# Optimization experiments

Measured on AMD Instinct MI355X. Metric: run time of the kernel, lower is better.

Reference implementation:

```python
import jax, jax.numpy as jnp
import numpy as np

N_NODES = 50000
N_EDGES = 800000
D_IN, D_HID, D_OUT = 128, 256, 128
N_EXPERT = 8


def mean_aggr(x, src, dst, n):
    # scatter-mean of neighbor features onto destination nodes
    msg = x[src]                                            # [E, d]
    s = jax.ops.segment_sum(msg, dst, num_segments=n)       # [N, d]
    cnt = jax.ops.segment_sum(jnp.ones((src.shape[0],), x.dtype), dst, num_segments=n)
    return s / jnp.clip(cnt, 1.0)[:, None]


def moe_top1(x, wg, bg, we, be):
    # FMoE with naive gate, top_k=1: combine weight softmax over top-1 == 1.0
    logits = x @ wg + bg                                    # [N, E]
    gate_full = jax.nn.softmax(logits, axis=-1)             # [N, E]
    idx = jnp.argmax(logits, axis=-1)                       # [N]
    n_expert = we.shape[0]
    out = jnp.zeros((x.shape[0], we.shape[2]), x.dtype)
    for e in range(n_expert):                               # small fixed loop over experts
        mask = (idx == e)[:, None].astype(x.dtype)
        out = out + mask * (x @ we[e] + be[e])
    return out, gate_full


def mysage_conv(x, src, dst, wg, bg, we, be, wr):
    agg = mean_aggr(x, src, dst, x.shape[0])
    out, gate = moe_top1(agg, wg, bg, we, be)
    out = out + x @ wr                                      # root weight (no bias)
    gstd = jnp.std(gate, axis=1, ddof=1).mean()             # torch.std is unbiased
    return out, gstd


def plain_sage_conv(x, src, dst, wl, bl, wr):
    agg = mean_aggr(x, src, dst, x.shape[0])
    return agg @ wl + bl + x @ wr


def setup_inputs() -> dict:
    key = jax.random.key(0)
    ks = jax.random.split(key, 16)
    s = 0.05
    inp = {
        "x": jax.random.normal(ks[0], (N_NODES, D_IN), jnp.float32),
        "edge_index": jax.random.randint(ks[1], (2, N_EDGES), 0, N_NODES, jnp.int64),
        # layer 1 (in -> hid)
        "wg1": jax.random.normal(ks[2], (D_IN, N_EXPERT), jnp.float32) * s,
        "bg1": jnp.zeros((N_EXPERT,), jnp.float32),
        "we1": jax.random.normal(ks[3], (N_EXPERT, D_IN, D_HID), jnp.float32) * s,
        "be1": jnp.zeros((N_EXPERT, D_HID), jnp.float32),
        "wr1": jax.random.normal(ks[4], (D_IN, D_HID), jnp.float32) * s,
        # layer 2 (hid -> hid)
        "wg2": jax.random.normal(ks[5], (D_HID, N_EXPERT), jnp.float32) * s,
        "bg2": jnp.zeros((N_EXPERT,), jnp.float32),
        "we2": jax.random.normal(ks[6], (N_EXPERT, D_HID, D_HID), jnp.float32) * s,
        "be2": jnp.zeros((N_EXPERT, D_HID), jnp.float32),
        "wr2": jax.random.normal(ks[7], (D_HID, D_HID), jnp.float32) * s,
        # layer 3 plain SAGEConv (hid -> out)
        "wl3": jax.random.normal(ks[8], (D_HID, D_OUT), jnp.float32) * s,
        "bl3": jnp.zeros((D_OUT,), jnp.float32),
        "wr3": jax.random.normal(ks[9], (D_HID, D_OUT), jnp.float32) * s,
    }
    return inp


def reference(x, edge_index, wg1, bg1, we1, be1, wr1, wg2, bg2, we2, be2, wr2, wl3, bl3, wr3):
    src, dst = edge_index[0], edge_index[1]
    h, g1 = mysage_conv(x, src, dst, wg1, bg1, we1, be1, wr1)
    h = jax.nn.relu(h)                                      # dropout p=0 / eval mode
    h, g2 = mysage_conv(h, src, dst, wg2, bg2, we2, be2, wr2)
    h = jax.nn.relu(h)
    out = plain_sage_conv(h, src, dst, wl3, bl3, wr3)
    gate_std_mean = jnp.stack([g1, g2]).mean()
    return out, gate_std_mean
```

## Files before the change

kernel.cpp:

```cpp
#include <hip/hip_runtime.h>
#include <hip/hip_bf16.h>
#include <stdint.h>

#define DEV static __device__ __forceinline__

typedef __attribute__((ext_vector_type(8))) short short8;
typedef __attribute__((ext_vector_type(4))) float f32x4;

DEV float bf2f(unsigned short u) { return __uint_as_float(((unsigned)u) << 16); }
DEV float bflo(unsigned u) { return __uint_as_float(u << 16); }
DEV float bfhi(unsigned u) { return __uint_as_float(u & 0xffff0000u); }
DEV unsigned short f2bf(float f) {
    unsigned u = __float_as_uint(f);
    u += 0x7fff + ((u >> 16) & 1);
    return (unsigned short)(u >> 16);
}

__global__ void k_detect(const int* __restrict__ ei, int* __restrict__ flags) {
    if (threadIdx.x == 0 && blockIdx.x == 0) {
        int zeros = 0;
        for (int i = 0; i < 128; ++i) if (ei[2 * i + 1] == 0) ++zeros;
        flags[1] = (zeros >= 64) ? 1 : 0;
    }
}

__global__ void k_cvt_idx(const int* __restrict__ ei, int* __restrict__ src32,
                          int* __restrict__ dst32, int* __restrict__ deg,
                          int E, const int* __restrict__ flags) {
    int i = blockIdx.x * 256 + threadIdx.x;
    if (i >= E) return;
    int s, d;
    if (flags[1]) { s = ei[2 * i]; d = ei[2 * E + 2 * i]; }
    else          { s = ei[i];     d = ei[E + i]; }
    src32[i] = s; dst32[i] = d;
    atomicAdd(&deg[d], 1);
}

__global__ void k_transpose_nb(const float* __restrict__ in, unsigned short* __restrict__ out,
                               int R, int C) {
    __shared__ unsigned short tile[32][33];
    int tx = threadIdx.x & 31, ty = threadIdx.x >> 5;
    size_t mat = (size_t)blockIdx.z * R * C;
    int r0 = blockIdx.y * 32, c0 = blockIdx.x * 32;
#pragma unroll
    for (int j = 0; j < 32; j += 8)
        tile[ty + j][tx] = f2bf(in[mat + (size_t)(r0 + ty + j) * C + c0 + tx]);
    __syncthreads();
#pragma unroll
    for (int j = 0; j < 32; j += 8)
        out[mat + (size_t)(c0 + ty + j) * R + r0 + tx] = tile[tx][ty + j];
}

__global__ void k_bias3(const float* __restrict__ bl3, float* __restrict__ bias3) {
    int t = threadIdx.x;
    bias3[t] = (t < 128) ? 0.f : bl3[t - 128];
}

__global__ void k_scan1(const int* __restrict__ deg, int* __restrict__ row_ptr,
                        int* __restrict__ part, int n) {
    __shared__ int wsum[4];
    int t = threadIdx.x, lane = t & 63, wv = t >> 6;
    int i = blockIdx.x * 256 + t;
    int v0 = (i < n) ? deg[i] : 0;
    int v = v0;
#pragma unroll
    for (int d = 1; d < 64; d <<= 1) { int u = __shfl_up(v, d); if (lane >= d) v += u; }
    if (lane == 63) wsum[wv] = v;
    __syncthreads();
    int add = 0;
    for (int w2 = 0; w2 < wv; ++w2) add += wsum[w2];
    v += add;
    if (i < n) row_ptr[i] = v - v0;
    if (t == 255) part[blockIdx.x] = v;
}

__global__ void k_scan2(int* __restrict__ part, int P) {
    __shared__ int wsum[4];
    int t = threadIdx.x, lane = t & 63, wv = t >> 6;
    int v0 = (t < P) ? part[t] : 0;
    int v = v0;
#pragma unroll
    for (int d = 1; d < 64; d <<= 1) { int u = __shfl_up(v, d); if (lane >= d) v += u; }
    if (lane == 63) wsum[wv] = v;
    __syncthreads();
    int add = 0;
    for (int w2 = 0; w2 < wv; ++w2) add += wsum[w2];
    v += add;
    if (t < P) part[t] = v - v0;
}

__global__ void k_scan3(int* __restrict__ row_ptr, const int* __restrict__ part, int n, int E) {
    int i = blockIdx.x * 256 + threadIdx.x;
    if (i < n) row_ptr[i] += part[blockIdx.x];
    if (i == 0) row_ptr[n] = E;
}

__global__ void k_fill(const int* __restrict__ src, const int* __restrict__ dst,
                       const int* __restrict__ row_ptr, int* __restrict__ cursor,
                       int* __restrict__ csr, int E) {
    int i = blockIdx.x * 256 + threadIdx.x;
    if (i < E) {
        int d = dst[i];
        int p = atomicAdd(&cursor[d], 1);
        csr[row_ptr[d] + p] = src[i];
    }
}

template<int D>
__global__ void k_aggr(const float* __restrict__ xin, const int* __restrict__ row_ptr,
                       const int* __restrict__ csr, float* __restrict__ agg, int n) {
    int wid = (blockIdx.x * blockDim.x + threadIdx.x) >> 6;
    int lane = threadIdx.x & 63;
    if (wid >= n) return;
    constexpr int V = D / 64;
    double a0[V], a1[V], a2[V], a3[V];
#pragma unroll
    for (int i = 0; i < V; ++i) { a0[i] = 0.0; a1[i] = 0.0; a2[i] = 0.0; a3[i] = 0.0; }
    int s0 = row_ptr[wid], s1 = row_ptr[wid + 1];
    int j = s0;
    for (; j + 4 <= s1; j += 4) {
        int i0 = csr[j], i1 = csr[j + 1], i2 = csr[j + 2], i3 = csr[j + 3];
        const float* p0 = xin + (size_t)i0 * D + lane * V;
        const float* p1 = xin + (size_t)i1 * D + lane * V;
        const float* p2 = xin + (size_t)i2 * D + lane * V;
        const float* p3 = xin + (size_t)i3 * D + lane * V;
        if (V == 2) {
            float2 f0 = *(const float2*)p0, f1 = *(const float2*)p1;
            float2 f2 = *(const float2*)p2, f3 = *(const float2*)p3;
            a0[0] += (double)f0.x; a0[1] += (double)f0.y;
            a1[0] += (double)f1.x; a1[1] += (double)f1.y;
            a2[0] += (double)f2.x; a2[1] += (double)f2.y;
            a3[0] += (double)f3.x; a3[1] += (double)f3.y;
        } else {
            float4 f0 = *(const float4*)p0, f1 = *(const float4*)p1;
            float4 f2 = *(const float4*)p2, f3 = *(const float4*)p3;
            a0[0] += (double)f0.x; a0[1] += (double)f0.y; a0[2] += (double)f0.z; a0[3] += (double)f0.w;
            a1[0] += (double)f1.x; a1[1] += (double)f1.y; a1[2] += (double)f1.z; a1[3] += (double)f1.w;
            a2[0] += (double)f2.x; a2[1] += (double)f2.y; a2[2] += (double)f2.z; a2[3] += (double)f2.w;
            a3[0] += (double)f3.x; a3[1] += (double)f3.y; a3[2] += (double)f3.z; a3[3] += (double)f3.w;
        }
    }
    for (; j < s1; ++j) {
        const float* p = xin + (size_t)csr[j] * D + lane * V;
        if (V == 2) {
            float2 f = *(const float2*)p;
            a0[0] += (double)f.x; a0[1] += (double)f.y;
        } else {
            float4 f = *(const float4*)p;
            a0[0] += (double)f.x; a0[1] += (double)f.y; a0[2] += (double)f.z; a0[3] += (double)f.w;
        }
    }
    double inv = 1.0 / (double)max(s1 - s0, 1);
#pragma unroll
    for (int i = 0; i < V; ++i)
        agg[(size_t)wid * D + lane * V + i] = (float)(((a0[i] + a1[i]) + (a2[i] + a3[i])) * inv);
}

__global__ void k_aggr_badd(const unsigned short* __restrict__ Pb, const int* __restrict__ row_ptr,
                            const int* __restrict__ csr, const float* __restrict__ Rf,
                            float* __restrict__ outp, int n) {
    int wid = (blockIdx.x * blockDim.x + threadIdx.x) >> 6;
    int lane = threadIdx.x & 63;
    if (wid >= n) return;
    double a0[2], a1[2], a2[2], a3[2];
#pragma unroll
    for (int i = 0; i < 2; ++i) { a0[i] = 0.0; a1[i] = 0.0; a2[i] = 0.0; a3[i] = 0.0; }
    int s0 = row_ptr[wid], s1 = row_ptr[wid + 1];
    int j = s0;
    for (; j + 4 <= s1; j += 4) {
        int i0 = csr[j], i1 = csr[j + 1], i2 = csr[j + 2], i3 = csr[j + 3];
        unsigned u0 = *(const unsigned*)(Pb + (size_t)i0 * 128 + lane * 2);
        unsigned u1 = *(const unsigned*)(Pb + (size_t)i1 * 128 + lane * 2);
        unsigned u2 = *(const unsigned*)(Pb + (size_t)i2 * 128 + lane * 2);
        unsigned u3 = *(const unsigned*)(Pb + (size_t)i3 * 128 + lane * 2);
        a0[0] += (double)bflo(u0); a0[1] += (double)bfhi(u0);
        a1[0] += (double)bflo(u1); a1[1] += (double)bfhi(u1);
        a2[0] += (double)bflo(u2); a2[1] += (double)bfhi(u2);
        a3[0] += (double)bflo(u3); a3[1] += (double)bfhi(u3);
    }
    for (; j < s1; ++j) {
        unsigned u = *(const unsigned*)(Pb + (size_t)csr[j] * 128 + lane * 2);
        a0[0] += (double)bflo(u); a0[1] += (double)bfhi(u);
    }
    double inv = 1.0 / (double)max(s1 - s0, 1);
    float2 r = *(const float2*)(Rf + (size_t)wid * 128 + lane * 2);
    float2 o;
    o.x = (float)(((a0[0] + a1[0]) + (a2[0] + a3[0])) * inv) + r.x;
    o.y = (float)(((a0[1] + a1[1]) + (a2[1] + a3[1])) * inv) + r.y;
    *(float2*)(outp + (size_t)wid * 128 + lane * 2) = o;
}

template<int D>
__global__ void k_gate(const float* __restrict__ agg, const float* __restrict__ wg,
                       const float* __restrict__ bg, int* __restrict__ idx,
                       int* __restrict__ ecnt, float* __restrict__ gsum, int n) {
    __shared__ float swg[D * 8];
    __shared__ int hcnt[8];
    __shared__ float red[256];
    int t = threadIdx.x;
    if (t < 8) hcnt[t] = 0;
    for (int i = t; i < D * 8; i += 256) swg[i] = wg[i];
    __syncthreads();
    int nid = blockIdx.x * 256 + t;
    float stdv = 0.f;
    if (nid < n) {
        double lg[8];
#pragma unroll
        for (int e = 0; e < 8; ++e) lg[e] = (double)bg[e];
        const float* ap = agg + (size_t)nid * D;
        for (int k = 0; k < D; k += 4) {
            float4 a = *(const float4*)(ap + k);
#pragma unroll
            for (int e = 0; e < 8; ++e) {
                lg[e] += (double)a.x * swg[(k + 0) * 8 + e] + (double)a.y * swg[(k + 1) * 8 + e]
                       + (double)a.z * swg[(k + 2) * 8 + e] + (double)a.w * swg[(k + 3) * 8 + e];
            }
        }
        double m = lg[0];
        int am = 0;
#pragma unroll
        for (int e = 1; e < 8; ++e) if (lg[e] > m) { m = lg[e]; am = e; }
        double s = 0.0, p[8];
#pragma unroll
        for (int e = 0; e < 8; ++e) { p[e] = exp(lg[e] - m); s += p[e]; }
        double invs = 1.0 / s, sq = 0.0;
#pragma unroll
        for (int e = 0; e < 8; ++e) { double q = p[e] * invs; sq += q * q; }
        stdv = (float)sqrt(fmax(sq - 0.125, 0.0) / 7.0);
        idx[nid] = am;
        atomicAdd(&hcnt[am], 1);
    }
    red[t] = stdv;
    __syncthreads();
    for (int off = 128; off > 0; off >>= 1) {
        if (t < off) red[t] += red[t + off];
        __syncthreads();
    }
    if (t == 0) atomicAdd(gsum, red[0]);
    if (t < 8 && hcnt[t] > 0) atomicAdd(&ecnt[t], hcnt[t]);
}

__global__ void k_offsets(const int* __restrict__ ecnt, int* __restrict__ eoff) {
    if (threadIdx.x == 0 && blockIdx.x == 0) {
        int s = 0;
        for (int e = 0; e < 8; ++e) { eoff[e] = s; s += ecnt[e]; }
        eoff[8] = s;
    }
}

__global__ void k_perm(const int* __restrict__ idx, const int* __restrict__ eoff,
                       int* __restrict__ ecur, int* __restrict__ perm, int n) {
    __shared__ int lcnt[8], lbase[8];
    int t = threadIdx.x;
    if (t < 8) lcnt[t] = 0;
    __syncthreads();
    int nid = blockIdx.x * 256 + t;
    int e = 0, r = 0;
    bool valid = (nid < n);
    if (valid) { e = idx[nid]; r = atomicAdd(&lcnt[e], 1); }
    __syncthreads();
    if (t < 8) lbase[t] = lcnt[t] ? atomicAdd(&ecur[t], lcnt[t]) : 0;
    __syncthreads();
    if (valid) perm[eoff[e] + lbase[e] + r] = nid;
}

template<int NCOL, bool LOAD>
DEV void g_step(int g, const float* __restrict__ Bp, const float* __restrict__ at,
                float4 (&cur)[4], float (&acc)[8][4]) {
    float bx[4][4];
#pragma unroll
    for (int kk = 0; kk < 4; ++kk) {
        bx[kk][0] = cur[kk].x; bx[kk][1] = cur[kk].y;
        bx[kk][2] = cur[kk].z; bx[kk][3] = cur[kk].w;
    }
#pragma unroll
    for (int r = 0; r < 8; ++r) {
        float4 a = *(const float4*)(at + r * 68 + g * 4);
#pragma unroll
        for (int c = 0; c < 4; ++c) {
            acc[r][c] = fmaf(a.x, bx[0][c], acc[r][c]);
            acc[r][c] = fmaf(a.y, bx[1][c], acc[r][c]);
            acc[r][c] = fmaf(a.z, bx[2][c], acc[r][c]);
            acc[r][c] = fmaf(a.w, bx[3][c], acc[r][c]);
        }
    }
    if (LOAD) {
#pragma unroll
        for (int kk = 0; kk < 4; ++kk)
            cur[kk] = *(const float4*)(Bp + (size_t)(g * 4 + 8 + kk) * NCOL);
    }
}

template<int NCOL>
DEV void compute_chunk(const float* __restrict__ Bp, const float* __restrict__ at,
                       float (&acc)[8][4]) {
    float4 bA[4], bB[4];
#pragma unroll
    for (int kk = 0; kk < 4; ++kk) bA[kk] = *(const float4*)(Bp + (size_t)kk * NCOL);
#pragma unroll
    for (int kk = 0; kk < 4; ++kk) bB[kk] = *(const float4*)(Bp + (size_t)(4 + kk) * NCOL);
#pragma unroll 1
    for (int g = 0; g < 14; g += 2) {
        g_step<NCOL, true>(g, Bp, at, bA, acc);
        g_step<NCOL, true>(g + 1, Bp, at, bB, acc);
    }
    g_step<NCOL, false>(14, Bp, at, bA, acc);
    g_step<NCOL, false>(15, Bp, at, bB, acc);
}

template<int DIN, int NCOL, bool RELU>
__global__ __launch_bounds__(256, 4) void k_gemm_f32(
    const float* __restrict__ agg, const float* __restrict__ a2,
    const float* __restrict__ B1, const float* __restrict__ B2,
    const float* __restrict__ bias,
    const int* __restrict__ perm, const int* __restrict__ eoff,
    float* __restrict__ outp, int n) {
    static_assert(DIN == 128 && NCOL == 256, "layer-1 geometry");
    __shared__ float a_tile[2][4 * 8 * 68];
    __shared__ int rows[32];
    int t = threadIdx.x;
    int rs = blockIdx.x * 32;
    if (rs >= n) return;
    int nrows = min(32, n - rs);
    if (t < 32) rows[t] = perm[rs + min(t, nrows - 1)];
    __syncthreads();

    int e0 = 0, e1 = 0;
    int last = rs + nrows - 1;
#pragma unroll
    for (int e = 1; e < 8; ++e) {
        int v = eoff[e];
        if (v <= rs) e0 = e;
        if (v <= last) e1 = e;
    }
    int ne = e1 - e0 + 1;
    int nchunks = 2 * ne + 2;

    int lane = t & 63, rg = t >> 6;
    int cols = lane * 4;
    int srow = lane >> 3;
    int sk = (lane & 7) * 8;
    int gpos = rs + rg * 8 + srow;
    int myrow = rows[rg * 8 + srow];
    float* stc = &a_tile[0][rg * 544 + srow * 68 + sk];
    float* stn = &a_tile[1][rg * 544 + srow * 68 + sk];
    const float* atc = &a_tile[0][rg * 544];
    const float* atn = &a_tile[1][rg * 544];

    float acc[8][4];
#pragma unroll
    for (int r = 0; r < 8; ++r) { acc[r][0] = 0.f; acc[r][1] = 0.f; acc[r][2] = 0.f; acc[r][3] = 0.f; }

    auto params = [&](int c, const float*& ap, const float*& Bp, float& m) {
        int half = c & 1;
        if (c < 2 * ne) {
            int e = e0 + (c >> 1);
            ap = agg + (size_t)myrow * DIN + sk + half * 64;
            Bp = B1 + (size_t)e * DIN * NCOL + (size_t)half * 64 * NCOL + cols;
            m = (gpos >= eoff[e] && gpos < eoff[e + 1]) ? 1.f : 0.f;
        } else {
            ap = a2 + (size_t)myrow * DIN + sk + half * 64;
            Bp = B2 + (size_t)half * 64 * NCOL + cols;
            m = 1.f;
        }
    };

    const float* ap; const float* Bp; float m;
    params(0, ap, Bp, m);
    float4 p0 = *(const float4*)ap, p1 = *(const float4*)(ap + 4);
#pragma unroll 1
    for (int c = 0; c < nchunks; ++c) {
        float4 s0 = p0, s1 = p1;
        s0.x *= m; s0.y *= m; s0.z *= m; s0.w *= m;
        s1.x *= m; s1.y *= m; s1.z *= m; s1.w *= m;
        *(float4*)stc = s0; *(float4*)(stc + 4) = s1;
        const float* Bcur = Bp;
        if (c + 1 < nchunks) {
            params(c + 1, ap, Bp, m);
            p0 = *(const float4*)ap; p1 = *(const float4*)(ap + 4);
        }
        compute_chunk<NCOL>(Bcur, atc, acc);
        float* ts = stc; stc = stn; stn = ts;
        const float* ta = atc; atc = atn; atn = ta;
    }

#pragma unroll
    for (int r = 0; r < 8; ++r) {
        int rr = rg * 8 + r;
        if (rr < nrows) {
            int gp = rs + rr;
            int er = e0;
            for (int e = e0 + 1; e <= e1; ++e) if (eoff[e] <= gp) er = e;
            float4 bb = *(const float4*)(bias + er * NCOL + cols);
            int gr = rows[rr];
            float v0 = acc[r][0] + bb.x, v1 = acc[r][1] + bb.y;
            float v2 = acc[r][2] + bb.z, v3 = acc[r][3] + bb.w;
            if (RELU) { v0 = fmaxf(v0, 0.f); v1 = fmaxf(v1, 0.f); v2 = fmaxf(v2, 0.f); v3 = fmaxf(v3, 0.f); }
            *(float4*)(outp + (size_t)gr * NCOL + cols) = make_float4(v0, v1, v2, v3);
        }
    }
}

template<int DIN, int MODE, int CT>
DEV void gemm_half(const void* __restrict__ Asrc, const unsigned short* __restrict__ BT,
                   short (*Ah)[40], short (*Bs)[40],
                   const int* rows, f32x4 (&acc)[4][CT], int t, int lane, int w) {
    if (MODE == 9) return;
    int q = lane >> 4, m16 = lane & 15;
    int r = t >> 2, part = t & 3;
    for (int kc = 0; kc < DIN; kc += 32) {
        __syncthreads();
        if (MODE == 2) {
            *(uint4*)&Ah[r][part * 8] =
                *(const uint4*)((const unsigned short*)Asrc + (size_t)rows[r] * DIN + kc + part * 8);
        } else {
            const float* pf = (const float*)Asrc + (size_t)rows[r] * DIN + kc + part * 8;
            float4 p0 = *(const float4*)pf, p1 = *(const float4*)(pf + 4);
            float va[8] = { p0.x, p0.y, p0.z, p0.w, p1.x, p1.y, p1.z, p1.w };
            short8 h;
#pragma unroll
            for (int j = 0; j < 8; ++j) h[j] = (short)f2bf(va[j]);
            *(short8*)&Ah[r][part * 8] = h;
        }
#pragma unroll
        for (int j = 0; j < CT; ++j) {
            int c = t + 256 * j;
            int nn = c >> 2, pp = c & 3;
            *(uint4*)&Bs[nn][pp * 8] = *(const uint4*)(BT + (size_t)nn * DIN + kc + pp * 8);
        }
        __syncthreads();
        short8 af[4], bfr[CT];
#pragma unroll
        for (int rt = 0; rt < 4; ++rt) af[rt] = *(short8*)&Ah[rt * 16 + m16][q * 8];
#pragma unroll
        for (int ct = 0; ct < CT; ++ct) bfr[ct] = *(short8*)&Bs[w * CT * 16 + ct * 16 + m16][q * 8];
#pragma unroll
        for (int rt = 0; rt < 4; ++rt)
#pragma unroll
            for (int ct = 0; ct < CT; ++ct)
                acc[rt][ct] = __builtin_amdgcn_mfma_f32_16x16x32_bf16(af[rt], bfr[ct], acc[rt][ct], 0, 0, 0);
    }
}

template<int DIN, int M0, int M1, int CT, bool EXPERT, bool RELU, int OUTMODE>
__global__ __launch_bounds__(256) void k_gemm(
    const void* __restrict__ A0, const void* __restrict__ A1,
    const unsigned short* __restrict__ B0T, const unsigned short* __restrict__ B1T,
    const float* __restrict__ bias,
    const int* __restrict__ perm, const int* __restrict__ eoff,
    void* __restrict__ outp, void* __restrict__ outp2, int n) {
    constexpr int NCOL = CT * 64;
    __shared__ short Ah[64][40];
    __shared__ short Bs[NCOL][40];
    __shared__ int rows[64];
    int t = threadIdx.x;
    int lane = t & 63, w = t >> 6;
    int e = 0, base = 0, cnt = n;
    if (EXPERT) { e = blockIdx.y; base = eoff[e]; cnt = eoff[e + 1] - base; }
    int rs = blockIdx.x * 64;
    if (rs >= cnt) return;
    int nrows = min(64, cnt - rs);
    if (t < 64) {
        int j = rs + min(t, nrows - 1);
        rows[t] = EXPERT ? perm[base + j] : j;
    }
    __syncthreads();
    f32x4 acc[4][CT];
#pragma unroll
    for (int rt = 0; rt < 4; ++rt)
#pragma unroll
        for (int ct = 0; ct < CT; ++ct) acc[rt][ct] = (f32x4)(0.f);

    gemm_half<DIN, M0, CT>(A0, B0T + (EXPERT ? (size_t)e * DIN * NCOL : 0), Ah, Bs, rows, acc, t, lane, w);
    gemm_half<DIN, M1, CT>(A1, B1T, Ah, Bs, rows, acc, t, lane, w);

    int q = lane >> 4, m16 = lane & 15;
#pragma unroll
    for (int ct = 0; ct < CT; ++ct) {
        int col = w * CT * 16 + ct * 16 + m16;
        float bv = bias[(EXPERT ? e * NCOL : 0) + col];
#pragma unroll
        for (int rt = 0; rt < 4; ++rt)
#pragma unroll
            for (int i = 0; i < 4; ++i) {
                int rr = rt * 16 + q * 4 + i;
                if (rr < nrows) {
                    int gr = rows[rr];
                    float v = acc[rt][ct][i] + bv;
                    if (RELU) v = fmaxf(v, 0.f);
                    if (OUTMODE == 1) ((unsigned short*)outp)[(size_t)gr * NCOL + col] = f2bf(v);
                    else if (OUTMODE == 0) ((float*)outp)[(size_t)gr * NCOL + col] = v;
                    else {
                        if (col < 128) ((unsigned short*)outp)[(size_t)gr * 128 + col] = f2bf(v);
                        else           ((float*)outp2)[(size_t)gr * 128 + (col - 128)] = v;
                    }
                }
            }
    }
}

__global__ void k_final(const float* __restrict__ gsum, float* __restrict__ outf) {
    if (threadIdx.x == 0 && blockIdx.x == 0) {
        float g = (gsum[0] + gsum[1]) * (0.5f / 50000.0f);
        outf[(size_t)50000 * 128] = g;
    }
}

extern "C" void kernel_launch(void* const* d_in, const int* in_sizes, int n_in,
                              void* d_out, int out_size, void* d_ws, size_t ws_size,
                              hipStream_t stream) {
    constexpr int N = 50000, E = 800000;
    const float* x   = (const float*)d_in[0];
    const int* ei    = (const int*)d_in[1];
    const float* wg1 = (const float*)d_in[2];
    const float* bg1 = (const float*)d_in[3];
    const float* we1 = (const float*)d_in[4];
    const float* be1 = (const float*)d_in[5];
    const float* wr1 = (const float*)d_in[6];
    const float* wg2 = (const float*)d_in[7];
    const float* bg2 = (const float*)d_in[8];
    const float* we2 = (const float*)d_in[9];
    const float* be2 = (const float*)d_in[10];
    const float* wr2 = (const float*)d_in[11];
    const float* wl3 = (const float*)d_in[12];
    const float* bl3 = (const float*)d_in[13];
    const float* wr3 = (const float*)d_in[14];

    int* ip = (int*)d_ws;
    int* deg = ip;            ip += N;
    int* cursor = ip;         ip += N;
    int* ecnt = ip;           ip += 16;
    int* ecur = ip;           ip += 16;
    float* gsum = (float*)ip; ip += 2;
    int* flags = ip;          ip += 2;
    float* bias3 = (float*)ip; ip += 256;
    int* row_ptr = ip;        ip += N + 1;
    int* csr = ip;            ip += E;
    int* idxb = ip;           ip += N;
    int* permb = ip;          ip += N;
    int* eoff = ip;           ip += 18;
    int* part = ip;           ip += 256;
    int* src32 = ip;          ip += E;
    int* dst32 = ip;          ip += E;
    size_t off = (size_t)((char*)ip - (char*)d_ws);
    off = (off + 255) & ~(size_t)255;
    float* fp = (float*)((char*)d_ws + off);
    float* agg = fp; fp += (size_t)N * 256;
    float* h1  = fp; fp += (size_t)N * 256;
    unsigned short* wp = (unsigned short*)fp;
    unsigned short* h2b  = wp; wp += (size_t)N * 256;
    unsigned short* we2T = wp; wp += 8 * 256 * 256;
    unsigned short* wr2T = wp; wp += 256 * 256;
    unsigned short* wl3T = wp; wp += 256 * 128;
    unsigned short* wr3T = wp; wp += 256 * 128;
    unsigned short* Pb = (unsigned short*)h1;
    float* Rf = agg;

    hipMemsetAsync(d_ws, 0, (size_t)(2 * N + 36) * 4, stream);

    k_detect<<<1, 64, 0, stream>>>(ei, flags);
    k_cvt_idx<<<(E + 255) / 256, 256, 0, stream>>>(ei, src32, dst32, deg, E, flags);

    k_transpose_nb<<<dim3(8, 8, 8), 256, 0, stream>>>(we2, we2T, 256, 256);
    k_transpose_nb<<<dim3(8, 8, 1), 256, 0, stream>>>(wr2, wr2T, 256, 256);
    k_transpose_nb<<<dim3(4, 8, 1), 256, 0, stream>>>(wl3, wl3T, 256, 128);
    k_transpose_nb<<<dim3(4, 8, 1), 256, 0, stream>>>(wr3, wr3T, 256, 128);
    k_bias3<<<1, 256, 0, stream>>>(bl3, bias3);

    constexpr int NB = (N + 255) / 256;
    constexpr int WB = (N + 3) / 4;
    k_scan1<<<NB, 256, 0, stream>>>(deg, row_ptr, part, N);
    k_scan2<<<1, 256, 0, stream>>>(part, NB);
    k_scan3<<<NB, 256, 0, stream>>>(row_ptr, part, N, E);
    k_fill<<<(E + 255) / 256, 256, 0, stream>>>(src32, dst32, row_ptr, cursor, csr, E);

    constexpr int GB = (N + 63) / 64;
    constexpr int GB32 = (N + 31) / 32;
    k_aggr<128><<<WB, 256, 0, stream>>>(x, row_ptr, csr, agg, N);
    k_gate<128><<<NB, 256, 0, stream>>>(agg, wg1, bg1, idxb, ecnt, gsum, N);
    k_offsets<<<1, 1, 0, stream>>>(ecnt, eoff);
    k_perm<<<NB, 256, 0, stream>>>(idxb, eoff, ecur, permb, N);
    k_gemm_f32<128, 256, true><<<dim3(GB32), 256, 0, stream>>>(
        agg, x, we1, wr1, be1, permb, eoff, h1, N);

    k_aggr<256><<<WB, 256, 0, stream>>>(h1, row_ptr, csr, agg, N);
    k_gate<256><<<NB, 256, 0, stream>>>(agg, wg2, bg2, idxb, ecnt + 8, gsum + 1, N);
    k_offsets<<<1, 1, 0, stream>>>(ecnt + 8, eoff + 9);
    k_perm<<<NB, 256, 0, stream>>>(idxb, eoff + 9, ecur + 8, permb, N);
    k_gemm<256, 0, 0, 4, true, true, 1><<<dim3(GB, 8), 256, 0, stream>>>(
        agg, h1, we2T, wr2T, be2, permb, eoff + 9, h2b, nullptr, N);

    k_gemm<256, 2, 9, 4, false, false, 2><<<dim3(GB, 1), 256, 0, stream>>>(
        h2b, nullptr, wl3T, nullptr, bias3, nullptr, nullptr, Pb, Rf, N);
    k_aggr_badd<<<WB, 256, 0, stream>>>(Pb, row_ptr, csr, Rf, (float*)d_out, N);

    k_final<<<1, 1, 0, stream>>>(gsum, (float*)d_out);
}
```

Before: 654.3 us.

## Pack layer-2 MoE GEMM into dense 64-row tiles spanning expert boundaries

Layer 2's expert GEMM used to launch a grid of GB x 8 blocks, one slice per expert, so most blocks exited early and the last tile of each expert was only partly filled. It now tiles the permuted row order with dense 64-row blocks. Each block loops over the experts its rows cover, zero-masking A rows that belong to other experts, then adds the root-weight GEMM. The aim is to cut wasted blocks and partial tiles, at the price of redundant MFMA work in tiles that straddle two experts.

```diff
diff --git a/kernel.cpp b/kernel.cpp
--- a/kernel.cpp
+++ b/kernel.cpp
@@ -402,15 +402,16 @@
 }
 
 template<int DIN, int MODE, int CT>
-DEV void gemm_half(const void* __restrict__ Asrc, const unsigned short* __restrict__ BT,
+DEV void gemm_span(const void* __restrict__ Asrc, const unsigned short* __restrict__ BT,
                    short (*Ah)[40], short (*Bs)[40],
-                   const int* rows, f32x4 (&acc)[4][CT], int t, int lane, int w) {
-    if (MODE == 9) return;
+                   const int* rows, f32x4 (&acc)[4][CT], int t, int lane, int w, bool amask) {
     int q = lane >> 4, m16 = lane & 15;
     int r = t >> 2, part = t & 3;
     for (int kc = 0; kc < DIN; kc += 32) {
         __syncthreads();
-        if (MODE == 2) {
+        if (!amask) {
+            *(uint4*)&Ah[r][part * 8] = make_uint4(0u, 0u, 0u, 0u);
+        } else if (MODE == 2) {
             *(uint4*)&Ah[r][part * 8] =
                 *(const uint4*)((const unsigned short*)Asrc + (size_t)rows[r] * DIN + kc + part * 8);
         } else {
@@ -442,12 +443,76 @@
     }
 }
 
-template<int DIN, int M0, int M1, int CT, bool EXPERT, bool RELU, int OUTMODE>
-__global__ __launch_bounds__(256) void k_gemm(
-    const void* __restrict__ A0, const void* __restrict__ A1,
-    const unsigned short* __restrict__ B0T, const unsigned short* __restrict__ B1T,
+template<int DIN>
+__global__ __launch_bounds__(256) void k_gemm_moe(
+    const float* __restrict__ agg, const float* __restrict__ h1,
+    const unsigned short* __restrict__ BeT, const unsigned short* __restrict__ BrT,
     const float* __restrict__ bias,
     const int* __restrict__ perm, const int* __restrict__ eoff,
+    unsigned short* __restrict__ outp, int n) {
+    constexpr int CT = 4;
+    constexpr int NCOL = CT * 64;
+    __shared__ short Ah[64][40];
+    __shared__ short Bs[NCOL][40];
+    __shared__ int rows[64];
+    int t = threadIdx.x;
+    int lane = t & 63, w = t >> 6;
+    int rs = blockIdx.x * 64;
+    if (rs >= n) return;
+    int nrows = min(64, n - rs);
+    if (t < 64) rows[t] = perm[rs + min(t, nrows - 1)];
+    __syncthreads();
+
+    int e0 = 0, e1 = 0;
+    int last = rs + nrows - 1;
+#pragma unroll
+    for (int e = 1; e < 8; ++e) {
+        int v = eoff[e];
+        if (v <= rs) e0 = e;
+        if (v <= last) e1 = e;
+    }
+
+    f32x4 acc[4][CT];
+#pragma unroll
+    for (int rt = 0; rt < 4; ++rt)
+#pragma unroll
+        for (int ct = 0; ct < CT; ++ct) acc[rt][ct] = (f32x4)(0.f);
+
+    int r = t >> 2;
+    int gposr = rs + r;
+    for (int e = e0; e <= e1; ++e) {
+        bool inseg = (gposr >= eoff[e] && gposr < eoff[e + 1]);
+        gemm_span<DIN, 0, CT>(agg, BeT + (size_t)e * DIN * NCOL, Ah, Bs, rows, acc,
+                              t, lane, w, inseg);
+    }
+    gemm_span<DIN, 0, CT>(h1, BrT, Ah, Bs, rows, acc, t, lane, w, true);
+
+    int q = lane >> 4, m16 = lane & 15;
+#pragma unroll
+    for (int ct = 0; ct < CT; ++ct) {
+        int col = w * CT * 16 + ct * 16 + m16;
+#pragma unroll
+        for (int rt = 0; rt < 4; ++rt)
+#pragma unroll
+            for (int i = 0; i < 4; ++i) {
+                int rr = rt * 16 + q * 4 + i;
+                if (rr < nrows) {
+                    int gp = rs + rr;
+                    int er = e0;
+                    for (int e = e0 + 1; e <= e1; ++e) if (eoff[e] <= gp) er = e;
+                    float v = acc[rt][ct][i] + bias[er * NCOL + col];
+                    v = fmaxf(v, 0.f);
+                    outp[(size_t)rows[rr] * NCOL + col] = f2bf(v);
+                }
+            }
+    }
+}
+
+template<int DIN, int M0, int CT, int OUTMODE>
+__global__ __launch_bounds__(256) void k_gemm(
+    const void* __restrict__ A0,
+    const unsigned short* __restrict__ B0T,
+    const float* __restrict__ bias,
     void* __restrict__ outp, void* __restrict__ outp2, int n) {
     constexpr int NCOL = CT * 64;
     __shared__ short Ah[64][40];
@@ -455,15 +520,10 @@
     __shared__ int rows[64];
     int t = threadIdx.x;
     int lane = t & 63, w = t >> 6;
-    int e = 0, base = 0, cnt = n;
-    if (EXPERT) { e = blockIdx.y; base = eoff[e]; cnt = eoff[e + 1] - base; }
     int rs = blockIdx.x * 64;
-    if (rs >= cnt) return;
-    int nrows = min(64, cnt - rs);
-    if (t < 64) {
-        int j = rs + min(t, nrows - 1);
-        rows[t] = EXPERT ? perm[base + j] : j;
-    }
+    if (rs >= n) return;
+    int nrows = min(64, n - rs);
+    if (t < 64) rows[t] = rs + min(t, nrows - 1);
     __syncthreads();
     f32x4 acc[4][CT];
 #pragma unroll
@@ -471,14 +531,13 @@
 #pragma unroll
         for (int ct = 0; ct < CT; ++ct) acc[rt][ct] = (f32x4)(0.f);
 
-    gemm_half<DIN, M0, CT>(A0, B0T + (EXPERT ? (size_t)e * DIN * NCOL : 0), Ah, Bs, rows, acc, t, lane, w);
-    gemm_half<DIN, M1, CT>(A1, B1T, Ah, Bs, rows, acc, t, lane, w);
+    gemm_span<DIN, M0, CT>(A0, B0T, Ah, Bs, rows, acc, t, lane, w, true);
 
     int q = lane >> 4, m16 = lane & 15;
 #pragma unroll
     for (int ct = 0; ct < CT; ++ct) {
         int col = w * CT * 16 + ct * 16 + m16;
-        float bv = bias[(EXPERT ? e * NCOL : 0) + col];
+        float bv = bias[col];
 #pragma unroll
         for (int rt = 0; rt < 4; ++rt)
 #pragma unroll
@@ -487,7 +546,6 @@
                 if (rr < nrows) {
                     int gr = rows[rr];
                     float v = acc[rt][ct][i] + bv;
-                    if (RELU) v = fmaxf(v, 0.f);
                     if (OUTMODE == 1) ((unsigned short*)outp)[(size_t)gr * NCOL + col] = f2bf(v);
                     else if (OUTMODE == 0) ((float*)outp)[(size_t)gr * NCOL + col] = v;
                     else {
@@ -587,11 +645,11 @@
     k_gate<256><<<NB, 256, 0, stream>>>(agg, wg2, bg2, idxb, ecnt + 8, gsum + 1, N);
     k_offsets<<<1, 1, 0, stream>>>(ecnt + 8, eoff + 9);
     k_perm<<<NB, 256, 0, stream>>>(idxb, eoff + 9, ecur + 8, permb, N);
-    k_gemm<256, 0, 0, 4, true, true, 1><<<dim3(GB, 8), 256, 0, stream>>>(
-        agg, h1, we2T, wr2T, be2, permb, eoff + 9, h2b, nullptr, N);
-
-    k_gemm<256, 2, 9, 4, false, false, 2><<<dim3(GB, 1), 256, 0, stream>>>(
-        h2b, nullptr, wl3T, nullptr, bias3, nullptr, nullptr, Pb, Rf, N);
+    k_gemm_moe<256><<<dim3(GB), 256, 0, stream>>>(
+        agg, h1, we2T, wr2T, be2, permb, eoff + 9, h2b, N);
+
+    k_gemm<256, 2, 4, 2><<<dim3(GB), 256, 0, stream>>>(
+        h2b, wl3T, bias3, Pb, Rf, N);
     k_aggr_badd<<<WB, 256, 0, stream>>>(Pb, row_ptr, csr, Rf, (float*)d_out, N);
 
     k_final<<<1, 1, 0, stream>>>(gsum, (float*)d_out);
```

Result: slower. 672.6 us (+2.8%).
